# Performance work log

Hardware: AMD Instinct MI355X
Metric: run time of the kernel (lower is better)

The kernel has to match this reference:

```python
import math
import jax, jax.numpy as jnp
import numpy as np

N_NODES = 4096
N_EDGES = 16384
N_EFEAT = 16384
L = 8          # mem_token
DIM = 512
HEAD = 8
NL = 2         # mid_num_layers
ROPE_THETA = 10000.0


def _rms(x, w, eps=1e-6):
    v = jnp.mean(jnp.square(x), axis=-1, keepdims=True)
    return x * jax.lax.rsqrt(v + eps) * w


def _rope_cos_sin(seq_len, d, theta):
    inv = 1.0 / (theta ** (jnp.arange(0, d, 2, dtype=jnp.float32) / d))
    f = jnp.outer(jnp.arange(seq_len, dtype=jnp.float32), inv)  # [L, d/2]
    emb = jnp.concatenate([f, f], axis=-1)                       # [L, d]
    return jnp.cos(emb), jnp.sin(emb)


def _rot_half(x):
    h = x.shape[-1] // 2
    return jnp.concatenate([-x[..., h:], x[..., :h]], axis=-1)


def setup_inputs() -> dict:
    key = jax.random.key(0)
    ks = jax.random.split(key, 12)
    s = 0.02
    return {
        "hidden_states": jax.random.normal(ks[0], (N_NODES + N_EFEAT, L * DIM), jnp.float32),
        "edge_index": jax.random.randint(ks[1], (2, N_EDGES), 0, N_NODES),
        "edge_map": jax.random.randint(ks[2], (N_EDGES,), 0, N_EFEAT),
        "num_node_feat": N_NODES,
        "W_qkv": jax.random.normal(ks[3], (NL, DIM, 3 * DIM), jnp.float32) * s,
        "W_e": jax.random.normal(ks[4], (NL, DIM, 2 * DIM), jnp.float32) * s,
        "W_o": jax.random.normal(ks[5], (NL, DIM, DIM), jnp.float32) * s,
        "x_norm_w": jnp.ones((NL, DIM), jnp.float32),
        "xe_norm_w": jnp.ones((NL, DIM), jnp.float32),
        "post_norm_w": jnp.ones((NL, DIM), jnp.float32),
        "ff_W1": jax.random.normal(ks[6], (NL, DIM, 2 * DIM), jnp.float32) * s,
        "ff_b1": jnp.zeros((NL, 2 * DIM), jnp.float32),
        "ff_W2": jax.random.normal(ks[7], (NL, 2 * DIM, DIM), jnp.float32) * s,
        "ff_b2": jnp.zeros((NL, DIM), jnp.float32),
    }


def reference(hidden_states, edge_index, edge_map, num_node_feat,
              W_qkv, W_e, W_o, x_norm_w, xe_norm_w, post_norm_w,
              ff_W1, ff_b1, ff_W2, ff_b2):
    n_layers, dim = W_qkv.shape[0], W_qkv.shape[1]
    n_tot = hidden_states.shape[0]
    seq = hidden_states.shape[1] // dim           # mem_token
    d = dim // HEAD                               # d_model per head
    N = int(num_node_feat)
    src, dst = edge_index[0], edge_index[1]
    cos, sin = _rope_cos_sin(seq, d, ROPE_THETA)
    cos = cos[None, :, None, :]   # [1, L, 1, d]
    sin = sin[None, :, None, :]
    inv_sqrt_d = 1.0 / math.sqrt(d)

    h = hidden_states.reshape(n_tot, seq, dim)
    for l in range(n_layers):
        x = h[:N]                        # [N, L, dim]
        xe = h[N:][edge_map]             # [E, L, dim]
        res = x
        xn = _rms(x, x_norm_w[l])
        xen = _rms(xe, xe_norm_w[l])
        q, k, v = jnp.split(jnp.einsum('nld,de->nle', xn, W_qkv[l]), 3, axis=-1)
        ek, ev = jnp.split(jnp.einsum('eld,df->elf', xen, W_e[l]), 2, axis=-1)
        # gather per-edge, fuse edge features into key/value
        qi = q[dst].reshape(-1, seq, HEAD, d)
        kj = (k[src] + ek).reshape(-1, seq, HEAD, d)
        vj = (v[src] + ev).reshape(-1, seq, HEAD, d)
        # rotary over memory-token positions
        qi = qi * cos + _rot_half(qi) * sin
        kj = kj * cos + _rot_half(kj) * sin
        alpha = jnp.einsum('elhd,elhd->elh', qi, kj) * inv_sqrt_d  # [E, L, H]
        # segment softmax over incoming edges of each destination node
        m = jax.ops.segment_max(alpha, dst, num_segments=N)
        m = jnp.where(jnp.isfinite(m), m, 0.0)
        a = jnp.exp(alpha - m[dst])
        s = jax.ops.segment_sum(a, dst, num_segments=N)
        a = a / (s[dst] + 1e-16)
        out_e = (vj * a[..., None]).reshape(-1, seq, dim)          # [E, L, dim]
        agg = jax.ops.segment_sum(out_e, dst, num_segments=N)      # [N, L, dim]
        out = res + jnp.einsum('nld,de->nle', agg, W_o[l])
        res2 = out
        o = _rms(out, post_norm_w[l])
        ff = jnp.einsum('nlf,fd->nld',
                        jax.nn.relu(jnp.einsum('nld,df->nlf', o, ff_W1[l]) + ff_b1[l]),
                        ff_W2[l]) + ff_b2[l]
        out = res2 + ff
        h = jnp.concatenate([out, h[N:]], axis=0)
    return h
```

## Files before the change

### kernel.cpp

```cpp
#include <hip/hip_runtime.h>

typedef unsigned short u16;
typedef unsigned int   u32;
typedef u16   u16x8 __attribute__((ext_vector_type(8)));
typedef __bf16 bf16x8 __attribute__((ext_vector_type(8)));
typedef float f32x4 __attribute__((ext_vector_type(4)));
typedef float f32x4v __attribute__((ext_vector_type(4)));

#define N_NODES 4096
#define N_EDGES 16384
#define N_EFEAT 16384
#define SEQ 8
#define DIM 512
#define NLAYER 2
#define NROWS_X (N_NODES*SEQ)
#define NROWS_E (N_EDGES*SEQ)

__device__ __forceinline__ float b2f(u16 u){ return __uint_as_float(((u32)u)<<16); }
__device__ __forceinline__ u16 f2b(float f){ u32 b=__float_as_uint(f); b += 0x7FFFu + ((b>>16)&1u); return (u16)(b>>16); }

__device__ __forceinline__ void gl16(const u16* g, u16* l) {
    __builtin_amdgcn_global_load_lds((const __attribute__((address_space(1))) void*)g,
                                     (__attribute__((address_space(3))) void*)l, 16, 0, 0);
}

__global__ void k_tf(const float* __restrict__ src, u16* __restrict__ dst,
                     const float* __restrict__ fold, int K, int N)
{
    int idx = blockIdx.x * 256 + threadIdx.x;
    if (idx >= K * N) return;
    int c = idx / N, j = idx - c * N;
    float v = src[idx];
    if (fold) v *= fold[c];
    dst[(size_t)j * K + c] = f2b(v);
}

__global__ void k_rowprep(const float* __restrict__ src, u16* __restrict__ dst,
                          float* __restrict__ scale)
{
    int row  = blockIdx.x * 4 + (threadIdx.x >> 6);
    int lane = threadIdx.x & 63;
    const float* p = src + (size_t)row * DIM;
    f32x4v v0 = *(const f32x4v*)(p + lane * 8);
    f32x4v v1 = *(const f32x4v*)(p + lane * 8 + 4);
    float ss = v0[0]*v0[0]+v0[1]*v0[1]+v0[2]*v0[2]+v0[3]*v0[3]
             + v1[0]*v1[0]+v1[1]*v1[1]+v1[2]*v1[2]+v1[3]*v1[3];
    #pragma unroll
    for (int d = 1; d < 64; d <<= 1) ss += __shfl_xor(ss, d);
    if (lane == 0) scale[row] = rsqrtf(ss / (float)DIM + 1e-6f);
    u16x8 o;
    #pragma unroll
    for (int i = 0; i < 4; ++i) o[i] = f2b(v0[i]);
    #pragma unroll
    for (int i = 0; i < 4; ++i) o[4+i] = f2b(v1[i]);
    *(u16x8*)(dst + (size_t)row * DIM + lane * 8) = o;
}

__global__ void k_mark(const int* __restrict__ emap, int* __restrict__ flag)
{
    int e = blockIdx.x * 256 + threadIdx.x;
    if (e < N_EDGES) flag[emap[e]] = 1;
}
__global__ void k_scanf(const int* __restrict__ flag, int* __restrict__ newid,
                        int* __restrict__ ulist, int* __restrict__ ucnt)
{
    __shared__ int part[256];
    int t = threadIdx.x;
    int base = t * 64;
    int loc[64]; int s = 0;
    #pragma unroll
    for (int i = 0; i < 64; ++i) { loc[i] = s; s += flag[base + i]; }
    part[t] = s; __syncthreads();
    for (int d = 1; d < 256; d <<= 1) {
        int v = (t >= d) ? part[t - d] : 0;
        __syncthreads();
        part[t] += v;
        __syncthreads();
    }
    int pre = (t == 0) ? 0 : part[t - 1];
    #pragma unroll
    for (int i = 0; i < 64; ++i) {
        int m = base + i;
        int id = pre + loc[i];
        newid[m] = id;
        if (flag[m]) ulist[id] = m;
    }
    if (t == 255) ucnt[0] = part[255];
}
__global__ void k_fidx(const int* __restrict__ emap, const int* __restrict__ newid,
                       int* __restrict__ fidx)
{
    int e = blockIdx.x * 256 + threadIdx.x;
    if (e < N_EDGES) fidx[e] = newid[emap[e]];
}
__global__ void k_featprep(const float* __restrict__ hidden, const int* __restrict__ ulist,
                           const int* __restrict__ ucnt,
                           u16* __restrict__ fbf, float* __restrict__ scale)
{
    int fr = blockIdx.x * 4 + (threadIdx.x >> 6);
    if (fr >= ucnt[0] * SEQ) return;
    int lane = threadIdx.x & 63;
    int j = fr >> 3, l = fr & 7;
    const float* p = hidden + ((size_t)(N_NODES + ulist[j]) * SEQ + l) * DIM;
    f32x4v v0 = *(const f32x4v*)(p + lane * 8);
    f32x4v v1 = *(const f32x4v*)(p + lane * 8 + 4);
    float ss = v0[0]*v0[0]+v0[1]*v0[1]+v0[2]*v0[2]+v0[3]*v0[3]
             + v1[0]*v1[0]+v1[1]*v1[1]+v1[2]*v1[2]+v1[3]*v1[3];
    #pragma unroll
    for (int d = 1; d < 64; d <<= 1) ss += __shfl_xor(ss, d);
    if (lane == 0) scale[fr] = rsqrtf(ss / (float)DIM + 1e-6f);
    u16x8 o;
    #pragma unroll
    for (int i = 0; i < 4; ++i) o[i] = f2b(v0[i]);
    #pragma unroll
    for (int i = 0; i < 4; ++i) o[4+i] = f2b(v1[i]);
    *(u16x8*)(fbf + (size_t)fr * DIM + lane * 8) = o;
}

__global__ void k_count(const int* __restrict__ dstA, int* __restrict__ cnt)
{
    int e = blockIdx.x * 256 + threadIdx.x;
    if (e < N_EDGES) atomicAdd(&cnt[dstA[e]], 1);
}
__global__ void k_scan(const int* __restrict__ cnt, int* __restrict__ off)
{
    __shared__ int part[256];
    int t = threadIdx.x;
    int base = t * 16;
    int loc[16]; int s = 0;
    #pragma unroll
    for (int i = 0; i < 16; ++i) { loc[i] = s; s += cnt[base + i]; }
    part[t] = s; __syncthreads();
    for (int d = 1; d < 256; d <<= 1) {
        int v = (t >= d) ? part[t - d] : 0;
        __syncthreads();
        part[t] += v;
        __syncthreads();
    }
    int pre = (t == 0) ? 0 : part[t - 1];
    #pragma unroll
    for (int i = 0; i < 16; ++i) off[base + i] = pre + loc[i];
    if (t == 255) off[N_NODES] = part[255];
}
__global__ void k_fill(const int* __restrict__ dstA, const int* __restrict__ off,
                       int* __restrict__ cur, int* __restrict__ elist)
{
    int e = blockIdx.x * 256 + threadIdx.x;
    if (e < N_EDGES) {
        int d = dstA[e];
        int pos = off[d] + atomicAdd(&cur[d], 1);
        elist[pos] = e;
    }
}

__global__ __launch_bounds__(256, 2) void k_gemm(
    const u16* __restrict__ A, const u16* __restrict__ B,
    int M, int N, int K, int gx, const int* __restrict__ mrows,
    const float* __restrict__ rowscale, const float* __restrict__ bias,
    int relu, const float* __restrict__ residual,
    float* __restrict__ outF, u16* __restrict__ outH)
{
    __shared__ u16 ldsA[2][128 * 32];
    __shared__ u16 ldsB[2][128 * 32];
    int tid  = threadIdx.x;
    int lane = tid & 63, wid = tid >> 6;

    int xcd  = blockIdx.x & 7;
    int i    = blockIdx.x >> 3;
    int colt = i % gx;
    int rowt = (i / gx) * 8 + xcd;
    int row0 = rowt * 128, col0 = colt * 128;
    if (mrows && row0 >= mrows[0] * SEQ) return;

    int r0 = wid * 32 + (lane >> 2);
    int r1 = r0 + 16;
    int ce0 = ((lane & 3) * 8) ^ (((r0 >> 1) & 3) << 3);
    int ce1 = ((lane & 3) * 8) ^ (((r1 >> 1) & 3) << 3);
    const u16* ga0 = A + (size_t)(row0 + r0) * K + ce0;
    const u16* ga1 = A + (size_t)(row0 + r1) * K + ce1;
    const u16* gb0 = B + (size_t)(col0 + r0) * K + ce0;
    const u16* gb1 = B + (size_t)(col0 + r1) * K + ce1;

    auto stage = [&](int buf, int kt) {
        int ko = kt * 32;
        gl16(ga0 + ko, &ldsA[buf][wid * 1024]);
        gl16(ga1 + ko, &ldsA[buf][wid * 1024 + 512]);
        gl16(gb0 + ko, &ldsB[buf][wid * 1024]);
        gl16(gb1 + ko, &ldsB[buf][wid * 1024 + 512]);
    };

    f32x4 acc[4][4];
    #pragma unroll
    for (int m = 0; m < 4; ++m)
        #pragma unroll
        for (int n = 0; n < 4; ++n) { f32x4 z = {0.f,0.f,0.f,0.f}; acc[m][n] = z; }

    int wr = wid >> 1, wc = wid & 1;
    int m15 = lane & 15, g = lane >> 4;
    int arow_l = wr * 64 + m15;
    int brow_l = wc * 64 + m15;
    int ksw = (g * 8) ^ (((m15 >> 1) & 3) << 3);

    int NT = K / 32;
    stage(0, 0);
    int cur = 0;
    for (int kt = 0; kt < NT; ++kt) {
        __syncthreads();
        if (kt + 1 < NT) stage(cur ^ 1, kt + 1);
        bf16x8 af[4], bfr[4];
        #pragma unroll
        for (int m = 0; m < 4; ++m)
            af[m] = *(const bf16x8*)&ldsA[cur][(arow_l + m * 16) * 32 + ksw];
        #pragma unroll
        for (int n = 0; n < 4; ++n)
            bfr[n] = *(const bf16x8*)&ldsB[cur][(brow_l + n * 16) * 32 + ksw];
        #pragma unroll
        for (int m = 0; m < 4; ++m)
            #pragma unroll
            for (int n = 0; n < 4; ++n)
                acc[m][n] = __builtin_amdgcn_mfma_f32_16x16x32_bf16(af[m], bfr[n], acc[m][n], 0, 0, 0);
        cur ^= 1;
    }

    #pragma unroll
    for (int m = 0; m < 4; ++m) {
        int rbase = row0 + wr * 64 + m * 16 + g * 4;
        #pragma unroll
        for (int n = 0; n < 4; ++n) {
            int col = col0 + wc * 64 + n * 16 + m15;
            #pragma unroll
            for (int j = 0; j < 4; ++j) {
                int row = rbase + j;
                float v = acc[m][n][j];
                if (rowscale) v *= rowscale[row];
                if (bias)     v += bias[col];
                if (relu)     v = fmaxf(v, 0.f);
                if (residual) v += residual[(size_t)row * N + col];
                if (outF) outF[(size_t)row * N + col] = v;
                else      outH[(size_t)row * N + col] = f2b(v);
            }
        }
    }
}

__global__ __launch_bounds__(256, 2) void k_attn(
    const u16* __restrict__ qkv, const u16* __restrict__ ekv,
    const int* __restrict__ srcA, const int* __restrict__ fidx,
    const int* __restrict__ off, const int* __restrict__ elist,
    u16* __restrict__ agg)
{
    int n = blockIdx.x;
    int t = threadIdx.x;
    int pair = t >> 2, sub = t & 3;
    int l = pair >> 3, hd = pair & 7;
    int doff = hd * 64 + sub * 16;

    size_t qrow = ((size_t)n * SEQ + l) * 1536;
    float qi[16];
    {
        u16x8 qa = *(const u16x8*)&qkv[qrow + doff];
        u16x8 qb = *(const u16x8*)&qkv[qrow + doff + 8];
        #pragma unroll
        for (int i = 0; i < 8; ++i) { qi[i] = b2f(qa[i]); qi[i + 8] = b2f(qb[i]); }
    }

    float mrun = -INFINITY, s = 0.f;
    float av[16];
    #pragma unroll
    for (int i = 0; i < 16; ++i) av[i] = 0.f;

    int e0 = off[n], e1 = off[n + 1];
    for (int ii = e0; ii < e1; ++ii) {
        int e = elist[ii];
        int es = srcA[e];
        size_t krow = ((size_t)es * SEQ + l) * 1536 + 512;
        size_t erow = ((size_t)fidx[e] * SEQ + l) * 1024;

        u16x8 ka = *(const u16x8*)&qkv[krow + doff];
        u16x8 kb = *(const u16x8*)&qkv[krow + doff + 8];
        u16x8 ea = *(const u16x8*)&ekv[erow + doff];
        u16x8 eb = *(const u16x8*)&ekv[erow + doff + 8];

        float dot = 0.f;
        #pragma unroll
        for (int i = 0; i < 8; ++i) {
            dot += qi[i]     * (b2f(ka[i]) + b2f(ea[i]));
            dot += qi[i + 8] * (b2f(kb[i]) + b2f(eb[i]));
        }
        dot += __shfl_xor(dot, 1);
        dot += __shfl_xor(dot, 2);
        float alpha = dot * 0.125f;

        float mn = fmaxf(mrun, alpha);
        float f = expf(mrun - mn);
        float p = expf(alpha - mn);
        s = s * f + p;

        u16x8 va  = *(const u16x8*)&qkv[krow + 512 + doff];
        u16x8 vb  = *(const u16x8*)&qkv[krow + 512 + doff + 8];
        u16x8 eva = *(const u16x8*)&ekv[erow + 512 + doff];
        u16x8 evb = *(const u16x8*)&ekv[erow + 512 + doff + 8];
        #pragma unroll
        for (int i = 0; i < 8; ++i) {
            av[i]     = av[i]     * f + p * (b2f(va[i]) + b2f(eva[i]));
            av[i + 8] = av[i + 8] * f + p * (b2f(vb[i]) + b2f(evb[i]));
        }
        mrun = mn;
    }

    float inv = 1.f / (s + 1e-16f);
    size_t orow = ((size_t)n * SEQ + l) * DIM + doff;
    #pragma unroll
    for (int i = 0; i < 16; ++i) agg[orow + i] = f2b(av[i] * inv);
}

extern "C" void kernel_launch(void* const* d_in, const int* in_sizes, int n_in,
                              void* d_out, int out_size, void* d_ws, size_t ws_size,
                              hipStream_t stream)
{
    const float* hidden = (const float*)d_in[0];
    const int*   eidx   = (const int*)d_in[1];
    const int*   srcA   = eidx;
    const int*   dstA   = eidx + N_EDGES;
    const int*   emap   = (const int*)d_in[2];
    const float* W_qkv  = (const float*)d_in[4];
    const float* W_e    = (const float*)d_in[5];
    const float* W_o    = (const float*)d_in[6];
    const float* xw     = (const float*)d_in[7];
    const float* xew    = (const float*)d_in[8];
    const float* pw     = (const float*)d_in[9];
    const float* W1     = (const float*)d_in[10];
    const float* b1     = (const float*)d_in[11];
    const float* W2     = (const float*)d_in[12];
    const float* b2     = (const float*)d_in[13];

    char* w = (char*)d_ws;
    auto alloc = [&](size_t bytes) { char* p = w; w += (bytes + 255) & ~(size_t)255; return p; };
    u16*  WtQKV  = (u16*)alloc((size_t)NLAYER * 1536 * 512 * 2);
    u16*  WtE    = (u16*)alloc((size_t)NLAYER * 1024 * 512 * 2);
    u16*  WtO    = (u16*)alloc((size_t)NLAYER * 512 * 512 * 2);
    u16*  Wt1    = (u16*)alloc((size_t)NLAYER * 1024 * 512 * 2);
    u16*  Wt2    = (u16*)alloc((size_t)NLAYER * 512 * 1024 * 2);
    float* s_x   = (float*)alloc((size_t)NROWS_X * 4);
    float* s_f   = (float*)alloc((size_t)NROWS_E * 4);
    float* s_post= (float*)alloc((size_t)NROWS_X * 4);
    int*  cnt    = (int*)alloc((N_NODES + 1) * 4);
    int*  off    = (int*)alloc((N_NODES + 1) * 4);
    int*  cur    = (int*)alloc(N_NODES * 4);
    int*  elist  = (int*)alloc(N_EDGES * 4);
    int*  flag   = (int*)alloc(N_EFEAT * 4);
    int*  newid  = (int*)alloc(N_EFEAT * 4);
    int*  ulist  = (int*)alloc(N_EFEAT * 4);
    int*  fidx   = (int*)alloc(N_EDGES * 4);
    int*  ucnt   = (int*)alloc(256);
    float* h_nodes = (float*)alloc((size_t)NROWS_X * DIM * 4);
    u16*  hn_bf  = (u16*)alloc((size_t)NROWS_X * DIM * 2);
    u16*  fbf    = (u16*)alloc((size_t)NROWS_E * DIM * 2);
    u16*  qkv    = (u16*)alloc((size_t)NROWS_X * 1536 * 2);
    u16*  aggB   = (u16*)alloc((size_t)NROWS_X * DIM * 2);
    float* out_buf = (float*)alloc((size_t)NROWS_X * DIM * 4);
    u16*  o_bf   = (u16*)alloc((size_t)NROWS_X * DIM * 2);
    u16*  ffmid  = (u16*)alloc((size_t)NROWS_X * 1024 * 2);
    u16*  ekv    = (u16*)((float*)d_out + (size_t)NROWS_X * DIM);

    for (int l = 0; l < NLAYER; ++l) {
        k_tf<<<(512*1536 + 255)/256, 256, 0, stream>>>(W_qkv + (size_t)l*512*1536, WtQKV + (size_t)l*1536*512, xw  + l*512, 512, 1536);
        k_tf<<<(512*1024 + 255)/256, 256, 0, stream>>>(W_e   + (size_t)l*512*1024, WtE   + (size_t)l*1024*512, xew + l*512, 512, 1024);
        k_tf<<<(512*512  + 255)/256, 256, 0, stream>>>(W_o   + (size_t)l*512*512,  WtO   + (size_t)l*512*512,  nullptr,    512, 512);
        k_tf<<<(512*1024 + 255)/256, 256, 0, stream>>>(W1    + (size_t)l*512*1024, Wt1   + (size_t)l*1024*512, pw  + l*512, 512, 1024);
        k_tf<<<(1024*512 + 255)/256, 256, 0, stream>>>(W2    + (size_t)l*1024*512, Wt2   + (size_t)l*512*1024, nullptr,    1024, 512);
    }
    hipMemsetAsync(flag, 0, N_EFEAT * 4, stream);
    k_mark<<<N_EDGES/256, 256, 0, stream>>>(emap, flag);
    k_scanf<<<1, 256, 0, stream>>>(flag, newid, ulist, ucnt);
    k_fidx<<<N_EDGES/256, 256, 0, stream>>>(emap, newid, fidx);
    k_featprep<<<NROWS_E/4, 256, 0, stream>>>(hidden, ulist, ucnt, fbf, s_f);
    hipMemsetAsync(cnt, 0, (N_NODES + 1) * 4, stream);
    hipMemsetAsync(cur, 0, N_NODES * 4, stream);
    k_count<<<N_EDGES/256, 256, 0, stream>>>(dstA, cnt);
    k_scan<<<1, 256, 0, stream>>>(cnt, off);
    k_fill<<<N_EDGES/256, 256, 0, stream>>>(dstA, off, cur, elist);

    for (int l = 0; l < NLAYER; ++l) {
        int last = (l == NLAYER - 1);
        const float* xsrc = (l == 0) ? hidden : h_nodes;
        k_rowprep<<<NROWS_X/4, 256, 0, stream>>>(xsrc, hn_bf, s_x);
        k_gemm<<<(NROWS_X/128)*(1536/128), 256, 0, stream>>>(hn_bf, WtQKV + (size_t)l*1536*512,
            NROWS_X, 1536, 512, 1536/128, nullptr, s_x, nullptr, 0, nullptr, nullptr, qkv);
        k_gemm<<<(NROWS_E/128)*(1024/128), 256, 0, stream>>>(fbf, WtE + (size_t)l*1024*512,
            NROWS_E, 1024, 512, 1024/128, ucnt, s_f, nullptr, 0, nullptr, nullptr, ekv);
        k_attn<<<N_NODES, 256, 0, stream>>>(qkv, ekv, srcA, fidx, off, elist, aggB);
        k_gemm<<<(NROWS_X/128)*(512/128), 256, 0, stream>>>(aggB, WtO + (size_t)l*512*512,
            NROWS_X, 512, 512, 512/128, nullptr, nullptr, nullptr, 0, xsrc, out_buf, nullptr);
        k_rowprep<<<NROWS_X/4, 256, 0, stream>>>(out_buf, o_bf, s_post);
        k_gemm<<<(NROWS_X/128)*(1024/128), 256, 0, stream>>>(o_bf, Wt1 + (size_t)l*1024*512,
            NROWS_X, 1024, 512, 1024/128, nullptr, s_post, b1 + l*1024, 1, nullptr, nullptr, ffmid);
        k_gemm<<<(NROWS_X/128)*(512/128), 256, 0, stream>>>(ffmid, Wt2 + (size_t)l*512*1024,
            NROWS_X, 512, 1024, 512/128, nullptr, nullptr, b2 + l*512, 0, out_buf,
            last ? (float*)d_out : h_nodes, nullptr);
    }

    hipMemcpyAsync((float*)d_out + (size_t)NROWS_X * DIM, hidden + (size_t)NROWS_X * DIM,
                   (size_t)N_EDGES * SEQ * DIM * 4, hipMemcpyDeviceToDevice, stream);
}
```

Before: 1.538 ms.

## Fuse RMSNorm statistics into GEMM epilogues and keep residual stream in bf16

Removes the per-layer rowprep kernels by accumulating row sums of squares in the producing GEMM's epilogue through shuffles and atomics. The consumer GEMM then applies rsqrt scaling from those sums. The residual stream (h_nodes, out_buf) is now stored only as bf16 instead of fp32 plus a bf16 copy, which halves its traffic. The cost is extra atomics in the epilogue and lower precision for the residual accumulation across layers.

```diff
diff --git a/kernel.cpp b/kernel.cpp
--- a/kernel.cpp
+++ b/kernel.cpp
@@ -36,7 +36,7 @@
 }
 
 __global__ void k_rowprep(const float* __restrict__ src, u16* __restrict__ dst,
-                          float* __restrict__ scale)
+                          float* __restrict__ ssout)
 {
     int row  = blockIdx.x * 4 + (threadIdx.x >> 6);
     int lane = threadIdx.x & 63;
@@ -47,7 +47,7 @@
              + v1[0]*v1[0]+v1[1]*v1[1]+v1[2]*v1[2]+v1[3]*v1[3];
     #pragma unroll
     for (int d = 1; d < 64; d <<= 1) ss += __shfl_xor(ss, d);
-    if (lane == 0) scale[row] = rsqrtf(ss / (float)DIM + 1e-6f);
+    if (lane == 0) ssout[row] = ss;
     u16x8 o;
     #pragma unroll
     for (int i = 0; i < 4; ++i) o[i] = f2b(v0[i]);
@@ -95,7 +95,7 @@
 }
 __global__ void k_featprep(const float* __restrict__ hidden, const int* __restrict__ ulist,
                            const int* __restrict__ ucnt,
-                           u16* __restrict__ fbf, float* __restrict__ scale)
+                           u16* __restrict__ fbf, float* __restrict__ ssout)
 {
     int fr = blockIdx.x * 4 + (threadIdx.x >> 6);
     if (fr >= ucnt[0] * SEQ) return;
@@ -108,7 +108,7 @@
              + v1[0]*v1[0]+v1[1]*v1[1]+v1[2]*v1[2]+v1[3]*v1[3];
     #pragma unroll
     for (int d = 1; d < 64; d <<= 1) ss += __shfl_xor(ss, d);
-    if (lane == 0) scale[fr] = rsqrtf(ss / (float)DIM + 1e-6f);
+    if (lane == 0) ssout[fr] = ss;
     u16x8 o;
     #pragma unroll
     for (int i = 0; i < 4; ++i) o[i] = f2b(v0[i]);
@@ -156,8 +156,8 @@
 __global__ __launch_bounds__(256, 2) void k_gemm(
     const u16* __restrict__ A, const u16* __restrict__ B,
     int M, int N, int K, int gx, const int* __restrict__ mrows,
-    const float* __restrict__ rowscale, const float* __restrict__ bias,
-    int relu, const float* __restrict__ residual,
+    const float* __restrict__ ssin, const float* __restrict__ bias, int relu,
+    const u16* __restrict__ resH, float* __restrict__ ssout,
     float* __restrict__ outF, u16* __restrict__ outH)
 {
     __shared__ u16 ldsA[2][128 * 32];
@@ -224,20 +224,30 @@
 
     #pragma unroll
     for (int m = 0; m < 4; ++m) {
-        int rbase = row0 + wr * 64 + m * 16 + g * 4;
-        #pragma unroll
-        for (int n = 0; n < 4; ++n) {
-            int col = col0 + wc * 64 + n * 16 + m15;
+        #pragma unroll
+        for (int j = 0; j < 4; ++j) {
+            int row = row0 + wr * 64 + m * 16 + g * 4 + j;
+            float sc = 0.f;
+            if (ssin) sc = rsqrtf(ssin[row] * (1.f / (float)DIM) + 1e-6f);
+            float ssa = 0.f;
             #pragma unroll
-            for (int j = 0; j < 4; ++j) {
-                int row = rbase + j;
+            for (int n = 0; n < 4; ++n) {
+                int col = col0 + wc * 64 + n * 16 + m15;
                 float v = acc[m][n][j];
-                if (rowscale) v *= rowscale[row];
-                if (bias)     v += bias[col];
-                if (relu)     v = fmaxf(v, 0.f);
-                if (residual) v += residual[(size_t)row * N + col];
+                if (ssin) v *= sc;
+                if (bias) v += bias[col];
+                if (relu) v = fmaxf(v, 0.f);
+                if (resH) v += b2f(resH[(size_t)row * N + col]);
                 if (outF) outF[(size_t)row * N + col] = v;
-                else      outH[(size_t)row * N + col] = f2b(v);
+                if (outH) outH[(size_t)row * N + col] = f2b(v);
+                ssa += v * v;
+            }
+            if (ssout) {
+                ssa += __shfl_xor(ssa, 1);
+                ssa += __shfl_xor(ssa, 2);
+                ssa += __shfl_xor(ssa, 4);
+                ssa += __shfl_xor(ssa, 8);
+                if (m15 == 0) atomicAdd(&ssout[row], ssa);
             }
         }
     }
@@ -341,9 +351,11 @@
     u16*  WtO    = (u16*)alloc((size_t)NLAYER * 512 * 512 * 2);
     u16*  Wt1    = (u16*)alloc((size_t)NLAYER * 1024 * 512 * 2);
     u16*  Wt2    = (u16*)alloc((size_t)NLAYER * 512 * 1024 * 2);
-    float* s_x   = (float*)alloc((size_t)NROWS_X * 4);
+    float* ssx0  = (float*)alloc((size_t)NROWS_X * 4);
+    float* ssx1  = (float*)alloc((size_t)NROWS_X * 4);
+    float* ssp0  = (float*)alloc((size_t)NROWS_X * 4);
+    float* ssp1  = (float*)alloc((size_t)NROWS_X * 4);
     float* s_f   = (float*)alloc((size_t)NROWS_E * 4);
-    float* s_post= (float*)alloc((size_t)NROWS_X * 4);
     int*  cnt    = (int*)alloc((N_NODES + 1) * 4);
     int*  off    = (int*)alloc((N_NODES + 1) * 4);
     int*  cur    = (int*)alloc(N_NODES * 4);
@@ -353,15 +365,15 @@
     int*  ulist  = (int*)alloc(N_EFEAT * 4);
     int*  fidx   = (int*)alloc(N_EDGES * 4);
     int*  ucnt   = (int*)alloc(256);
-    float* h_nodes = (float*)alloc((size_t)NROWS_X * DIM * 4);
-    u16*  hn_bf  = (u16*)alloc((size_t)NROWS_X * DIM * 2);
+    u16*  hb     = (u16*)alloc((size_t)NROWS_X * DIM * 2);
+    u16*  ob     = (u16*)alloc((size_t)NROWS_X * DIM * 2);
     u16*  fbf    = (u16*)alloc((size_t)NROWS_E * DIM * 2);
     u16*  qkv    = (u16*)alloc((size_t)NROWS_X * 1536 * 2);
     u16*  aggB   = (u16*)alloc((size_t)NROWS_X * DIM * 2);
-    float* out_buf = (float*)alloc((size_t)NROWS_X * DIM * 4);
-    u16*  o_bf   = (u16*)alloc((size_t)NROWS_X * DIM * 2);
     u16*  ffmid  = (u16*)alloc((size_t)NROWS_X * 1024 * 2);
     u16*  ekv    = (u16*)((float*)d_out + (size_t)NROWS_X * DIM);
+    float* ssx[2] = { ssx0, ssx1 };
+    float* ssp[2] = { ssp0, ssp1 };
 
     for (int l = 0; l < NLAYER; ++l) {
         k_tf<<<(512*1536 + 255)/256, 256, 0, stream>>>(W_qkv + (size_t)l*512*1536, WtQKV + (size_t)l*1536*512, xw  + l*512, 512, 1536);
@@ -370,6 +382,9 @@
         k_tf<<<(512*1024 + 255)/256, 256, 0, stream>>>(W1    + (size_t)l*512*1024, Wt1   + (size_t)l*1024*512, pw  + l*512, 512, 1024);
         k_tf<<<(1024*512 + 255)/256, 256, 0, stream>>>(W2    + (size_t)l*1024*512, Wt2   + (size_t)l*512*1024, nullptr,    1024, 512);
     }
+    hipMemsetAsync(ssx1, 0, NROWS_X * 4, stream);
+    hipMemsetAsync(ssp0, 0, NROWS_X * 4, stream);
+    hipMemsetAsync(ssp1, 0, NROWS_X * 4, stream);
     hipMemsetAsync(flag, 0, N_EFEAT * 4, stream);
     k_mark<<<N_EDGES/256, 256, 0, stream>>>(emap, flag);
     k_scanf<<<1, 256, 0, stream>>>(flag, newid, ulist, ucnt);
@@ -380,24 +395,29 @@
     k_count<<<N_EDGES/256, 256, 0, stream>>>(dstA, cnt);
     k_scan<<<1, 256, 0, stream>>>(cnt, off);
     k_fill<<<N_EDGES/256, 256, 0, stream>>>(dstA, off, cur, elist);
+    k_rowprep<<<NROWS_X/4, 256, 0, stream>>>(hidden, hb, ssx0);
 
     for (int l = 0; l < NLAYER; ++l) {
         int last = (l == NLAYER - 1);
-        const float* xsrc = (l == 0) ? hidden : h_nodes;
-        k_rowprep<<<NROWS_X/4, 256, 0, stream>>>(xsrc, hn_bf, s_x);
-        k_gemm<<<(NROWS_X/128)*(1536/128), 256, 0, stream>>>(hn_bf, WtQKV + (size_t)l*1536*512,
-            NROWS_X, 1536, 512, 1536/128, nullptr, s_x, nullptr, 0, nullptr, nullptr, qkv);
+        k_gemm<<<(NROWS_X/128)*(1536/128), 256, 0, stream>>>(hb, WtQKV + (size_t)l*1536*512,
+            NROWS_X, 1536, 512, 1536/128, nullptr,
+            ssx[l], nullptr, 0, nullptr, nullptr, nullptr, qkv);
         k_gemm<<<(NROWS_E/128)*(1024/128), 256, 0, stream>>>(fbf, WtE + (size_t)l*1024*512,
-            NROWS_E, 1024, 512, 1024/128, ucnt, s_f, nullptr, 0, nullptr, nullptr, ekv);
+            NROWS_E, 1024, 512, 1024/128, ucnt,
+            s_f, nullptr, 0, nullptr, nullptr, nullptr, ekv);
         k_attn<<<N_NODES, 256, 0, stream>>>(qkv, ekv, srcA, fidx, off, elist, aggB);
         k_gemm<<<(NROWS_X/128)*(512/128), 256, 0, stream>>>(aggB, WtO + (size_t)l*512*512,
-            NROWS_X, 512, 512, 512/128, nullptr, nullptr, nullptr, 0, xsrc, out_buf, nullptr);
-        k_rowprep<<<NROWS_X/4, 256, 0, stream>>>(out_buf, o_bf, s_post);
-        k_gemm<<<(NROWS_X/128)*(1024/128), 256, 0, stream>>>(o_bf, Wt1 + (size_t)l*1024*512,
-            NROWS_X, 1024, 512, 1024/128, nullptr, s_post, b1 + l*1024, 1, nullptr, nullptr, ffmid);
+            NROWS_X, 512, 512, 512/128, nullptr,
+            nullptr, nullptr, 0, hb, ssp[l], nullptr, ob);
+        k_gemm<<<(NROWS_X/128)*(1024/128), 256, 0, stream>>>(ob, Wt1 + (size_t)l*1024*512,
+            NROWS_X, 1024, 512, 1024/128, nullptr,
+            ssp[l], b1 + l*1024, 1, nullptr, nullptr, nullptr, ffmid);
         k_gemm<<<(NROWS_X/128)*(512/128), 256, 0, stream>>>(ffmid, Wt2 + (size_t)l*512*1024,
-            NROWS_X, 512, 1024, 512/128, nullptr, nullptr, b2 + l*512, 0, out_buf,
-            last ? (float*)d_out : h_nodes, nullptr);
+            NROWS_X, 512, 1024, 512/128, nullptr,
+            nullptr, b2 + l*512, 0, ob,
+            last ? nullptr : ssx[1],
+            last ? (float*)d_out : nullptr,
+            last ? nullptr : hb);
     }
 
     hipMemcpyAsync((float*)d_out + (size_t)NROWS_X * DIM, hidden + (size_t)NROWS_X * DIM,
```

New measurement: 1.342 ms. 1.15x faster.
